# Kernel optimization log

Measured on AMD Instinct MI355X. Metric: run time of the kernel, lower is better.

Reference implementation:

```python
import jax, jax.numpy as jnp
import numpy as np

B, S, H = 1, 2048, 2048
HD, NQ, NKV = 128, 16, 4
FFH = 8192
EPS = 1e-5
ROPE_BASE = 10000.0
SOFTMAX_CAP = 50.0
CLIP_L, CLIP_R = 0.0, 1.0


def setup_inputs() -> dict:
    key = jax.random.key(0)
    ks = jax.random.split(key, 10)
    std = 0.02
    return {
        "x": jax.random.normal(ks[0], (B, S, H), dtype=jnp.float32),
        "attn_norm_w": jax.random.uniform(ks[1], (H,), minval=-1.0, maxval=1.0, dtype=jnp.float32),
        "mlp_norm_w": jax.random.uniform(ks[2], (H,), minval=-1.0, maxval=1.0, dtype=jnp.float32),
        "wq": jax.random.normal(ks[3], (H, NQ * HD), dtype=jnp.float32) * std,
        "wk": jax.random.normal(ks[4], (H, NKV * HD), dtype=jnp.float32) * std,
        "wv": jax.random.normal(ks[5], (H, NKV * HD), dtype=jnp.float32) * std,
        "wo": jax.random.normal(ks[6], (NQ * HD, H), dtype=jnp.float32) * std,
        "w_gate": jax.random.normal(ks[7], (H, FFH), dtype=jnp.float32) * std,
        "w_up": jax.random.normal(ks[8], (H, FFH), dtype=jnp.float32) * std,
        "w_down": jax.random.normal(ks[9], (FFH, H), dtype=jnp.float32) * std,
    }


def _rms_norm(x, w):
    # GroupRMSNorm with group_size=None -> whole hidden dim
    var = jnp.mean(jnp.square(x), axis=-1, keepdims=True)
    return x * jax.lax.rsqrt(var + EPS) * w


def _rope_cos_sin(seq_len, dim):
    inv_freq = 1.0 / (ROPE_BASE ** (jnp.arange(0, dim, 2, dtype=jnp.float32) / dim))
    t = jnp.arange(seq_len, dtype=jnp.float32)
    freqs = jnp.outer(t, inv_freq)                      # [S, dim/2]
    emb = jnp.concatenate([freqs, freqs], axis=-1)      # [S, dim]
    return jnp.cos(emb), jnp.sin(emb)


def _apply_rope(x, cos, sin):
    # x: [B, S, h, d]; rotate-half (LLaMA-style)
    d = x.shape[-1]
    x1, x2 = x[..., : d // 2], x[..., d // 2 :]
    rot = jnp.concatenate([-x2, x1], axis=-1)
    return x * cos[None, :, None, :] + rot * sin[None, :, None, :]


def _qk_norm(x):
    # per-head RMS norm over head_dim (qk_norm_group_size == head_dim), unit weight
    var = jnp.mean(jnp.square(x), axis=-1, keepdims=True)
    return x * jax.lax.rsqrt(var + EPS)


def reference(x, attn_norm_w, mlp_norm_w, wq, wk, wv, wo, w_gate, w_up, w_down):
    # ---- attention sub-layer ----
    h = _rms_norm(x, attn_norm_w)                                     # [B,S,H]
    q = (h @ wq).reshape(B, S, NQ, HD)
    k = (h @ wk).reshape(B, S, NKV, HD)
    v = (h @ wv).reshape(B, S, NKV, HD)

    cos, sin = _rope_cos_sin(S, HD)
    q = _apply_rope(q, cos, sin)
    k = _apply_rope(k, cos, sin)

    q = _qk_norm(q)
    k = _qk_norm(k)

    # GQA: expand kv heads to match q heads
    rep = NQ // NKV
    k = jnp.repeat(k, rep, axis=2)                                    # [B,S,NQ,HD]
    v = jnp.repeat(v, rep, axis=2)

    scale = 1.0 / jnp.sqrt(jnp.float32(HD))
    scores = jnp.einsum("bshd,bthd->bhst", q, k) * scale              # [B,NQ,S,S]
    # softmax cap: cap * tanh(s / cap)
    scores = SOFTMAX_CAP * jnp.tanh(scores / SOFTMAX_CAP)
    causal = jnp.tril(jnp.ones((S, S), dtype=bool))
    scores = jnp.where(causal[None, None], scores, -jnp.inf)
    p = jax.nn.softmax(scores, axis=-1)
    # clip range (l, r): clamp(p * (r - l) + l, 0, 1)
    p = jnp.clip(p * (CLIP_R - CLIP_L) + CLIP_L, 0.0, 1.0)
    o = jnp.einsum("bhst,bthd->bshd", p, v).reshape(B, S, NQ * HD)
    x = x + o @ wo

    # ---- MLP sub-layer (gated SiLU) ----
    h2 = _rms_norm(x, mlp_norm_w)
    mlp_out = (jax.nn.silu(h2 @ w_gate) * (h2 @ w_up)) @ w_down
    return x + mlp_out
```

## Files before the change

kernel.cpp:

```cpp
#include <hip/hip_runtime.h>

typedef __bf16 bf16;
typedef __bf16 bf16x4 __attribute__((ext_vector_type(4)));
typedef __bf16 bf16x8 __attribute__((ext_vector_type(8)));
typedef float f32x4 __attribute__((ext_vector_type(4)));

#define GLP16(gp, lp) __builtin_amdgcn_global_load_lds( \
    (const __attribute__((address_space(1))) void*)(gp), \
    (__attribute__((address_space(3))) void*)(lp), 16, 0, 0)

__device__ __forceinline__ f32x4 mfma16(bf16x8 a, bf16x8 b, f32x4 c) {
    return __builtin_amdgcn_mfma_f32_16x16x32_bf16(a, b, c, 0, 0, 0);
}

__global__ __launch_bounds__(256) void k_rmsnorm(const float* __restrict__ x,
        const float* __restrict__ w, bf16* __restrict__ out) {
    const int H = 2048;
    size_t row = blockIdx.x;
    const float* xr = x + row * H;
    int base = threadIdx.x * 8;
    float4 a = *(const float4*)(xr + base);
    float4 b = *(const float4*)(xr + base + 4);
    float ss = a.x*a.x + a.y*a.y + a.z*a.z + a.w*a.w
             + b.x*b.x + b.y*b.y + b.z*b.z + b.w*b.w;
#pragma unroll
    for (int m = 32; m > 0; m >>= 1) ss += __shfl_xor(ss, m);
    __shared__ float red[4];
    if ((threadIdx.x & 63) == 0) red[threadIdx.x >> 6] = ss;
    __syncthreads();
    float tot = red[0] + red[1] + red[2] + red[3];
    float rs = rsqrtf(tot * (1.0f / H) + 1e-5f);
    float4 wa = *(const float4*)(w + base);
    float4 wb = *(const float4*)(w + base + 4);
    bf16x8 ov;
    ov[0] = (bf16)(a.x * rs * wa.x); ov[1] = (bf16)(a.y * rs * wa.y);
    ov[2] = (bf16)(a.z * rs * wa.z); ov[3] = (bf16)(a.w * rs * wa.w);
    ov[4] = (bf16)(b.x * rs * wb.x); ov[5] = (bf16)(b.y * rs * wb.y);
    ov[6] = (bf16)(b.z * rs * wb.z); ov[7] = (bf16)(b.w * rs * wb.w);
    *(bf16x8*)(out + row * H + base) = ov;
}

__global__ __launch_bounds__(256) void k_convT(const float* __restrict__ W,
        bf16* __restrict__ Wt, int K, int N) {
    __shared__ float t[32][33];
    int k0 = blockIdx.x * 32, n0 = blockIdx.y * 32;
    int tx = threadIdx.x, ty = threadIdx.y;
#pragma unroll
    for (int i = 0; i < 4; i++)
        t[ty + i * 8][tx] = W[(size_t)(k0 + ty + i * 8) * N + n0 + tx];
    __syncthreads();
#pragma unroll
    for (int i = 0; i < 4; i++)
        Wt[(size_t)(n0 + ty + i * 8) * K + k0 + tx] = (bf16)t[tx][ty + i * 8];
}

__global__ __launch_bounds__(256) void k_transpose(const bf16* __restrict__ in,
        bf16* __restrict__ out, int R, int C) {
    __shared__ bf16 t[32][33];
    int r0 = blockIdx.x * 32, c0 = blockIdx.y * 32;
    int tx = threadIdx.x & 31, ty = threadIdx.x >> 5;
#pragma unroll
    for (int i = 0; i < 4; i++)
        t[ty + i * 8][tx] = in[(size_t)(r0 + ty + i * 8) * C + c0 + tx];
    __syncthreads();
#pragma unroll
    for (int i = 0; i < 4; i++)
        out[(size_t)(c0 + ty + i * 8) * R + r0 + tx] = t[tx][ty + i * 8];
}

template<int EPI>
__global__ __launch_bounds__(512, 2) void k_gemm4(const bf16* __restrict__ A,
        const bf16* __restrict__ Bt, void* __restrict__ outp,
        const void* __restrict__ aux, int M, int N, int K, int ksplit) {
    extern __shared__ char lds[];
    const int tid = threadIdx.x, wave = tid >> 6, lane = tid & 63;
    const int lr = lane & 15, kg = lane >> 4;
    const int wm = wave >> 2, wn = wave & 3;
    const int bn = blockIdx.x, bm = blockIdx.y, split = blockIdx.z;
    const int row0 = bm * 256, col0 = bn * 256;
    const int kbeg = split * ksplit;
    const int NT = ksplit >> 6;
    const size_t K2 = (size_t)K * 2;
    const int xorm = (lr & 7) << 4;

    char* const A0 = lds;
    char* const A1 = lds + 32768;
    char* const B0 = lds + 65536;
    char* const B1 = lds + 98304;

    size_t soff[2];
#pragma unroll
    for (int s = 0; s < 2; s++) {
        int d = s * 8192 + tid * 16;
        int rh = d >> 7, c = d & 127;
        soff[s] = (size_t)rh * K2 + (c ^ ((rh & 7) << 4));
    }
    const char* Ab = (const char*)A + ((size_t)row0 * K + kbeg) * 2;
    const char* Bb = (const char*)Bt + ((size_t)col0 * K + kbeg) * 2;

    auto stA = [&](int t, int mh) {
        const char* src = Ab + (size_t)(mh * 128) * K2 + (size_t)t * 128;
        char* dst = lds + (t & 1) * 32768 + mh * 16384 + wave * 1024;
        GLP16(src + soff[0], dst);
        GLP16(src + soff[1], dst + 8192);
    };
    auto stB = [&](int t, int nh) {
        const char* src = Bb + (size_t)(nh * 128) * K2 + (size_t)t * 128;
        char* dst = lds + 65536 + (t & 1) * 32768 + nh * 16384 + wave * 1024;
        GLP16(src + soff[0], dst);
        GLP16(src + soff[1], dst + 8192);
    };

    f32x4 acc[8][4];
#pragma unroll
    for (int m = 0; m < 8; m++)
#pragma unroll
        for (int n = 0; n < 4; n++) acc[m][n] = (f32x4){0, 0, 0, 0};

    bf16x8 a[8], c0[4], c1[4];
    auto rdA = [&](const char* base, int mh) {
#pragma unroll
        for (int mi = 0; mi < 4; mi++)
#pragma unroll
            for (int kk = 0; kk < 2; kk++) {
                int rh = wm * 64 + mi * 16 + lr;
                int c = (kk * 64 + kg * 16) ^ xorm;
                a[mi * 2 + kk] = *(const bf16x8*)(base + mh * 16384 + rh * 128 + c);
            }
    };
    auto rdB = [&](const char* base, int nh, bf16x8 (&b)[4]) {
#pragma unroll
        for (int nj = 0; nj < 2; nj++)
#pragma unroll
            for (int kk = 0; kk < 2; kk++) {
                int rh = wn * 32 + nj * 16 + lr;
                int c = (kk * 64 + kg * 16) ^ xorm;
                b[nj * 2 + kk] = *(const bf16x8*)(base + nh * 16384 + rh * 128 + c);
            }
    };
    auto mm = [&](int mh, int nh, bf16x8 (&b)[4]) {
#pragma unroll
        for (int mi = 0; mi < 4; mi++)
#pragma unroll
            for (int nj = 0; nj < 2; nj++)
#pragma unroll
                for (int kk = 0; kk < 2; kk++)
                    acc[mh * 4 + mi][nh * 2 + nj] =
                        mfma16(a[mi * 2 + kk], b[nj * 2 + kk],
                               acc[mh * 4 + mi][nh * 2 + nj]);
    };

#define SYNCMM \
    __builtin_amdgcn_sched_barrier(0); \
    __builtin_amdgcn_s_barrier(); \
    asm volatile("s_waitcnt lgkmcnt(0)" ::: "memory"); \
    __builtin_amdgcn_sched_barrier(0); \
    __builtin_amdgcn_s_setprio(1);
#define ENDPH \
    __builtin_amdgcn_s_setprio(0); \
    __builtin_amdgcn_sched_barrier(0); \
    __builtin_amdgcn_s_barrier();

    stA(0, 0); stB(0, 0); stB(0, 1); stA(0, 1);
    stA(1, 0); stB(1, 0); stB(1, 1);
    asm volatile("s_waitcnt vmcnt(6)" ::: "memory");
    __builtin_amdgcn_s_barrier();

    const int NIT = NT >> 1;
    for (int it = 0; it < NIT; ++it) {
        const int t = it * 2;
        const bool more = (t + 2 < NT);
        rdA(A0, 0); rdB(B0, 0, c0);
        stA(t + 1, 1);
        SYNCMM; mm(0, 0, c0); ENDPH;
        rdB(B0, 1, c1);
        if (more) stA(t + 2, 0);
        SYNCMM; mm(0, 1, c1); ENDPH;
        rdA(A0, 1);
        if (more) stB(t + 2, 0);
        SYNCMM; mm(1, 1, c1); ENDPH;
        if (more) stB(t + 2, 1);
        __builtin_amdgcn_sched_barrier(0);
        __builtin_amdgcn_s_barrier();
        __builtin_amdgcn_s_setprio(1);
        mm(1, 0, c0);
        __builtin_amdgcn_s_setprio(0);
        if (more) asm volatile("s_waitcnt vmcnt(6)" ::: "memory");
        else      asm volatile("s_waitcnt vmcnt(0)" ::: "memory");
        __builtin_amdgcn_sched_barrier(0);
        __builtin_amdgcn_s_barrier();
        rdA(A1, 0); rdB(B1, 0, c0);
        if (more) stA(t + 2, 1);
        SYNCMM; mm(0, 0, c0); ENDPH;
        rdB(B1, 1, c1);
        if (t + 3 < NT) stA(t + 3, 0);
        SYNCMM; mm(0, 1, c1); ENDPH;
        rdA(A1, 1);
        if (t + 3 < NT) stB(t + 3, 0);
        SYNCMM; mm(1, 1, c1); ENDPH;
        if (t + 3 < NT) stB(t + 3, 1);
        __builtin_amdgcn_sched_barrier(0);
        __builtin_amdgcn_s_barrier();
        __builtin_amdgcn_s_setprio(1);
        mm(1, 0, c0);
        __builtin_amdgcn_s_setprio(0);
        if (more) asm volatile("s_waitcnt vmcnt(6)" ::: "memory");
        __builtin_amdgcn_sched_barrier(0);
        __builtin_amdgcn_s_barrier();
    }
#undef SYNCMM
#undef ENDPH

#pragma unroll
    for (int mi = 0; mi < 8; mi++)
#pragma unroll
        for (int ni = 0; ni < 4; ni++)
#pragma unroll
            for (int r = 0; r < 4; r++) {
                size_t row = row0 + (mi >> 2) * 128 + wm * 64 + (mi & 3) * 16 + kg * 4 + r;
                size_t col = col0 + (ni >> 1) * 128 + wn * 32 + (ni & 1) * 16 + lr;
                size_t idx = row * N + col;
                float vv = acc[mi][ni][r];
                if (EPI == 0) {
                    ((bf16*)outp)[idx] = (bf16)vv;
                } else if (EPI == 2) {
                    float g = (float)((const bf16*)aux)[idx];
                    float sg = g / (1.0f + __expf(-g));
                    ((bf16*)outp)[idx] = (bf16)(sg * vv);
                } else {
                    ((float*)outp)[(size_t)split * M * N + idx] = vv;
                }
            }
}

__global__ __launch_bounds__(256) void k_reduce(const float* __restrict__ parts,
        const float* __restrict__ resid, float* __restrict__ out,
        int ns, size_t n4) {
    size_t i = (size_t)blockIdx.x * 256 + threadIdx.x;
    if (i >= n4) return;
    float4 acc = ((const float4*)resid)[i];
    for (int s = 0; s < ns; s++) {
        float4 p = ((const float4*)(parts + (size_t)s * n4 * 4))[i];
        acc.x += p.x; acc.y += p.y; acc.z += p.z; acc.w += p.w;
    }
    ((float4*)out)[i] = acc;
}

__global__ __launch_bounds__(256) void k_reduce_rms(const float* __restrict__ parts,
        const float* __restrict__ resid, const float* __restrict__ w,
        float* __restrict__ x2, bf16* __restrict__ hb, int ns) {
    const int H = 2048;
    size_t row = blockIdx.x;
    int base = threadIdx.x * 8;
    const float* rr = resid + row * H + base;
    float4 a = *(const float4*)rr;
    float4 b = *(const float4*)(rr + 4);
    for (int s = 0; s < ns; s++) {
        const float* pp = parts + (size_t)s * H * 2048 + row * H + base;
        float4 pa = *(const float4*)pp;
        float4 pb = *(const float4*)(pp + 4);
        a.x += pa.x; a.y += pa.y; a.z += pa.z; a.w += pa.w;
        b.x += pb.x; b.y += pb.y; b.z += pb.z; b.w += pb.w;
    }
    *(float4*)(x2 + row * H + base) = a;
    *(float4*)(x2 + row * H + base + 4) = b;
    float ss = a.x*a.x + a.y*a.y + a.z*a.z + a.w*a.w
             + b.x*b.x + b.y*b.y + b.z*b.z + b.w*b.w;
#pragma unroll
    for (int m = 32; m > 0; m >>= 1) ss += __shfl_xor(ss, m);
    __shared__ float red[4];
    if ((threadIdx.x & 63) == 0) red[threadIdx.x >> 6] = ss;
    __syncthreads();
    float tot = red[0] + red[1] + red[2] + red[3];
    float rs = rsqrtf(tot * (1.0f / H) + 1e-5f);
    float4 wa = *(const float4*)(w + base);
    float4 wb = *(const float4*)(w + base + 4);
    bf16x8 ov;
    ov[0] = (bf16)(a.x * rs * wa.x); ov[1] = (bf16)(a.y * rs * wa.y);
    ov[2] = (bf16)(a.z * rs * wa.z); ov[3] = (bf16)(a.w * rs * wa.w);
    ov[4] = (bf16)(b.x * rs * wb.x); ov[5] = (bf16)(b.y * rs * wb.y);
    ov[6] = (bf16)(b.z * rs * wb.z); ov[7] = (bf16)(b.w * rs * wb.w);
    *(bf16x8*)(hb + row * H + base) = ov;
}

__global__ __launch_bounds__(256) void k_qkvfin(const float* __restrict__ parts,
        bf16* __restrict__ qb, bf16* __restrict__ kb, bf16* __restrict__ vb) {
    int s = blockIdx.x;
    int col = blockIdx.y * 1024 + threadIdx.x * 4;
    const float* p0 = parts + (size_t)s * 3072 + col;
    const float* p1 = p0 + (size_t)2048 * 3072;
    float4 a = *(const float4*)p0;
    float4 b = *(const float4*)p1;
    a.x += b.x; a.y += b.y; a.z += b.z; a.w += b.w;
    bf16x4 o;
    o[0] = (bf16)a.x; o[1] = (bf16)a.y; o[2] = (bf16)a.z; o[3] = (bf16)a.w;
    if (col < 2048)      *(bf16x4*)(qb + (size_t)s * 2048 + col) = o;
    else if (col < 2560) *(bf16x4*)(kb + (size_t)s * 512 + col - 2048) = o;
    else                 *(bf16x4*)(vb + (size_t)s * 512 + col - 2560) = o;
}

__global__ __launch_bounds__(64) void k_rope(bf16* __restrict__ q,
        bf16* __restrict__ k) {
    int s = blockIdx.x, hid = blockIdx.y, lane = threadIdx.x;
    bf16* p;
    if (hid < 16) p = q + (size_t)s * 2048 + hid * 128;
    else          p = k + (size_t)s * 512 + (hid - 16) * 128;
    float x1 = (float)p[lane], x2 = (float)p[lane + 64];
    float f = exp2f((float)lane * -0.2076205059304601f);
    float sn, cs;
    sincosf((float)s * f, &sn, &cs);
    float o1 = x1 * cs - x2 * sn;
    float o2 = x2 * cs + x1 * sn;
    float ss = o1 * o1 + o2 * o2;
#pragma unroll
    for (int m = 32; m > 0; m >>= 1) ss += __shfl_xor(ss, m);
    float rs = rsqrtf(ss * (1.0f / 128.0f) + 1e-5f);
    p[lane] = (bf16)(o1 * rs);
    p[lane + 64] = (bf16)(o2 * rs);
}

__global__ __launch_bounds__(256) void k_attn(const bf16* __restrict__ qg,
        const bf16* __restrict__ kgl, const bf16* __restrict__ vtg,
        bf16* __restrict__ og) {
    extern __shared__ char alds[];
    int pi = blockIdx.x, h = blockIdx.y, kvh = h >> 2;
    int tid = threadIdx.x, wave = tid >> 6, lane = tid & 63;
    int lr = lane & 15, kgrp = lane >> 4;

    int rowQ[4], colQ[4], rowV[4], colV[4];
#pragma unroll
    for (int j = 0; j < 4; j++) {
        int p = j * 4096 + wave * 1024 + lane * 16;
        int ps = p ^ (((p >> 8) & 7) << 4);
        rowQ[j] = ps >> 8; colQ[j] = ps & 255;
        int pv = p ^ (((p >> 7) & 7) << 4);
        rowV[j] = pv >> 7; colV[j] = pv & 127;
    }

    const float C1 = 0.08838834764831845f / 50.0f;
    const float L2E50 = 72.13475204444817f;

#pragma unroll 1
    for (int half = 0; half < 2; ++half) {
        int qt = half ? (31 - pi) : pi;
        int nt = qt + 1;

#pragma unroll
        for (int j = 0; j < 4; j++)
            GLP16((const char*)qg + (size_t)(qt * 64 + rowQ[j]) * 4096 + h * 256 + colQ[j],
                  alds + j * 4096 + wave * 1024);
        for (int t = 0; t < 2 && t < nt; t++) {
#pragma unroll
            for (int j = 0; j < 4; j++)
                GLP16((const char*)kgl + (size_t)(t * 64 + rowQ[j]) * 1024 + kvh * 256 + colQ[j],
                      alds + 16384 + t * 16384 + j * 4096 + wave * 1024);
#pragma unroll
            for (int j = 0; j < 4; j++)
                GLP16((const char*)vtg + (size_t)(kvh * 128 + rowV[j]) * 4096 + t * 128 + colV[j],
                      alds + 49152 + t * 16384 + j * 4096 + wave * 1024);
        }
        if (nt > 1) asm volatile("s_waitcnt vmcnt(8)" ::: "memory");
        else        asm volatile("s_waitcnt vmcnt(0)" ::: "memory");
        __builtin_amdgcn_s_barrier();

        bf16x8 qf[4];
#pragma unroll
        for (int c = 0; c < 4; c++) {
            int b = (wave * 16 + lr) * 256 + c * 64 + kgrp * 16;
            qf[c] = *(const bf16x8*)(alds + (b ^ (((b >> 8) & 7) << 4)));
        }
        f32x4 accO[8];
#pragma unroll
        for (int n = 0; n < 8; n++) accO[n] = (f32x4){0, 0, 0, 0};
        float lsum[4] = {0, 0, 0, 0};
        int qrow = qt * 64 + wave * 16 + kgrp * 4;

        for (int kt = 0; kt < nt; kt++) {
            int buf = kt & 1;
            const char* Kb = alds + 16384 + buf * 16384;
            const char* Vb = alds + 49152 + buf * 16384;
            char* Pb = alds + 81920;
#pragma unroll
            for (int j = 0; j < 4; j++) {
                f32x4 s = {0, 0, 0, 0};
#pragma unroll
                for (int c = 0; c < 4; c++) {
                    int b = (j * 16 + lr) * 256 + c * 64 + kgrp * 16;
                    bf16x8 kf = *(const bf16x8*)(Kb + (b ^ (((b >> 8) & 7) << 4)));
                    s = mfma16(qf[c], kf, s);
                }
                int key = kt * 64 + j * 16 + lr;
#pragma unroll
                for (int r = 0; r < 4; r++) {
                    float y = s[r] * C1;
                    float y2 = y * y;
                    float u = fmaf(y2, 0.13333333f, -0.33333333f);
                    u = fmaf(y2, u, 1.0f);
                    float t5 = y * u;
                    float pe = fmaf(t5, L2E50, -L2E50);
                    float pv = (key <= qrow + r) ? exp2f(pe) : 0.0f;
                    lsum[r] += pv;
                    int wb = (wave * 16 + kgrp * 4 + r) * 128 + (j * 16 + lr) * 2;
                    *(bf16*)(Pb + (wb ^ (((wb >> 7) & 7) << 4))) = (bf16)pv;
                }
            }
            bf16x8 pf[2];
#pragma unroll
            for (int ks2 = 0; ks2 < 2; ks2++) {
                int b = (wave * 16 + lr) * 128 + ks2 * 64 + kgrp * 16;
                pf[ks2] = *(const bf16x8*)(Pb + (b ^ (((b >> 7) & 7) << 4)));
            }
#pragma unroll
            for (int n = 0; n < 8; n++)
#pragma unroll
                for (int ks2 = 0; ks2 < 2; ks2++) {
                    int b = (n * 16 + lr) * 128 + ks2 * 64 + kgrp * 16;
                    bf16x8 vf = *(const bf16x8*)(Vb + (b ^ (((b >> 7) & 7) << 4)));
                    accO[n] = mfma16(pf[ks2], vf, accO[n]);
                }
            __builtin_amdgcn_s_barrier();
            bool more = (kt + 2 < nt);
            if (more) {
                int t = kt + 2;
#pragma unroll
                for (int j = 0; j < 4; j++)
                    GLP16((const char*)kgl + (size_t)(t * 64 + rowQ[j]) * 1024 + kvh * 256 + colQ[j],
                          alds + 16384 + buf * 16384 + j * 4096 + wave * 1024);
#pragma unroll
                for (int j = 0; j < 4; j++)
                    GLP16((const char*)vtg + (size_t)(kvh * 128 + rowV[j]) * 4096 + t * 128 + colV[j],
                          alds + 49152 + buf * 16384 + j * 4096 + wave * 1024);
            }
            if (kt + 1 < nt) {
                if (more) asm volatile("s_waitcnt vmcnt(8)" ::: "memory");
                else      asm volatile("s_waitcnt vmcnt(0)" ::: "memory");
                __builtin_amdgcn_s_barrier();
            }
        }
#pragma unroll
        for (int r = 0; r < 4; r++) {
            float t = lsum[r];
            t += __shfl_xor(t, 1); t += __shfl_xor(t, 2);
            t += __shfl_xor(t, 4); t += __shfl_xor(t, 8);
            lsum[r] = t;
        }
#pragma unroll
        for (int n = 0; n < 8; n++)
#pragma unroll
            for (int r = 0; r < 4; r++) {
                size_t row = qt * 64 + wave * 16 + kgrp * 4 + r;
                og[row * 2048 + h * 128 + n * 16 + lr] = (bf16)(accO[n][r] / lsum[r]);
            }
    }
}

extern "C" void kernel_launch(void* const* d_in, const int* in_sizes, int n_in,
                              void* d_out, int out_size, void* d_ws, size_t ws_size,
                              hipStream_t stream) {
    const float* x      = (const float*)d_in[0];
    const float* attn_w = (const float*)d_in[1];
    const float* mlp_w  = (const float*)d_in[2];
    const float* wq     = (const float*)d_in[3];
    const float* wk     = (const float*)d_in[4];
    const float* wv     = (const float*)d_in[5];
    const float* wo     = (const float*)d_in[6];
    const float* wgate  = (const float*)d_in[7];
    const float* wup    = (const float*)d_in[8];
    const float* wdown  = (const float*)d_in[9];
    float* out = (float*)d_out;
    char* ws = (char*)d_ws;

    const size_t MB = 1024 * 1024;
    bf16* W1  = (bf16*)(ws + 0);
    bf16* W2  = (bf16*)(ws + 32 * MB);
    bf16* W3  = (bf16*)(ws + 64 * MB);
    bf16* hb  = (bf16*)(ws + 96 * MB);
    bf16* qb  = (bf16*)(ws + 104 * MB);
    bf16* kb  = (bf16*)(ws + 112 * MB);
    bf16* vb  = (bf16*)(ws + 114 * MB);
    bf16* ob  = (bf16*)(ws + 116 * MB);
    float* x2 = (float*)(ws + 124 * MB);
    bf16* gb  = (bf16*)(ws + 140 * MB);
    bf16* vt  = (bf16*)(ws + 0);
    float* parts = (float*)(ws + 0);
    float* partsq = (float*)(ws + 116 * MB);

    const int LDS4 = 131072;
    hipFuncSetAttribute((const void*)&k_gemm4<0>,
        hipFuncAttributeMaxDynamicSharedMemorySize, LDS4);
    hipFuncSetAttribute((const void*)&k_gemm4<2>,
        hipFuncAttributeMaxDynamicSharedMemorySize, LDS4);
    hipFuncSetAttribute((const void*)&k_gemm4<3>,
        hipFuncAttributeMaxDynamicSharedMemorySize, LDS4);
    const int LDSA = 90112;
    hipFuncSetAttribute((const void*)&k_attn,
        hipFuncAttributeMaxDynamicSharedMemorySize, LDSA);

    dim3 cb(32, 8);
    const size_t n4 = (size_t)2048 * 2048 / 4;

    k_rmsnorm<<<2048, 256, 0, stream>>>(x, attn_w, hb);
    k_convT<<<dim3(64, 64), cb, 0, stream>>>(wq, W1, 2048, 2048);
    k_convT<<<dim3(64, 16), cb, 0, stream>>>(wk, W1 + 4194304, 2048, 512);
    k_convT<<<dim3(64, 16), cb, 0, stream>>>(wv, W1 + 5242880, 2048, 512);
    k_gemm4<3><<<dim3(12, 8, 2), 512, LDS4, stream>>>(hb, W1, partsq, nullptr,
                                                      2048, 3072, 2048, 1024);
    k_qkvfin<<<dim3(2048, 3), 256, 0, stream>>>(partsq, qb, kb, vb);
    k_transpose<<<dim3(64, 16), 256, 0, stream>>>(vb, vt, 2048, 512);
    k_rope<<<dim3(2048, 20), 64, 0, stream>>>(qb, kb);
    k_attn<<<dim3(16, 16), 256, LDSA, stream>>>(qb, kb, vt, ob);
    k_convT<<<dim3(64, 64), cb, 0, stream>>>(wo, W2, 2048, 2048);
    k_gemm4<3><<<dim3(8, 8, 2), 512, LDS4, stream>>>(ob, W2, parts, nullptr,
                                                     2048, 2048, 2048, 1024);
    k_reduce_rms<<<2048, 256, 0, stream>>>(parts, x, mlp_w, x2, hb, 2);
    k_convT<<<dim3(64, 256), cb, 0, stream>>>(wgate, W1, 2048, 8192);
    k_gemm4<0><<<dim3(32, 8, 1), 512, LDS4, stream>>>(hb, W1, gb, nullptr,
                                                      2048, 8192, 2048, 2048);
    k_convT<<<dim3(64, 256), cb, 0, stream>>>(wup, W2, 2048, 8192);
    k_gemm4<2><<<dim3(32, 8, 1), 512, LDS4, stream>>>(hb, W2, gb, gb,
                                                      2048, 8192, 2048, 2048);
    k_convT<<<dim3(256, 64), cb, 0, stream>>>(wdown, W3, 8192, 2048);
    k_gemm4<3><<<dim3(8, 8, 4), 512, LDS4, stream>>>(gb, W3, parts, nullptr,
                                                     2048, 2048, 8192, 2048);
    k_reduce<<<4096, 256, 0, stream>>>(parts, x2, out, 4, n4);
}
```

Baseline: 473.6 us.

## Fuse gate/up GEMMs via interleaved weights, simplify GEMM barriers, widen rope blocks

Gate and up weights are transposed into one interleaved matrix, so a single GEMM produces both projections and the epilogue pairs adjacent lanes to apply SiLU(gate)*up. This removes the second GEMM's separate A-pass and the bf16 gate round-trip through memory. The GEMM main loop drops the per-phase lgkmcnt waits and sched barriers in favour of plain compiler-fenced barriers, which relies on the compiler inserting the needed LDS waits. The output-projection split-K goes from 2 to 4, and rope runs four heads per 256-thread block instead of one head per 64-thread block.

```diff
diff --git a/kernel.cpp b/kernel.cpp
--- a/kernel.cpp
+++ b/kernel.cpp
@@ -41,7 +41,7 @@
 }
 
 __global__ __launch_bounds__(256) void k_convT(const float* __restrict__ W,
-        bf16* __restrict__ Wt, int K, int N) {
+        bf16* __restrict__ Wt, int K, int N, int rmul, int roff) {
     __shared__ float t[32][33];
     int k0 = blockIdx.x * 32, n0 = blockIdx.y * 32;
     int tx = threadIdx.x, ty = threadIdx.y;
@@ -51,7 +51,8 @@
     __syncthreads();
 #pragma unroll
     for (int i = 0; i < 4; i++)
-        Wt[(size_t)(n0 + ty + i * 8) * K + k0 + tx] = (bf16)t[tx][ty + i * 8];
+        Wt[((size_t)(n0 + ty + i * 8) * rmul + roff) * K + k0 + tx] =
+            (bf16)t[tx][ty + i * 8];
 }
 
 __global__ __launch_bounds__(256) void k_transpose(const bf16* __restrict__ in,
@@ -69,7 +70,7 @@
 }
 
 template<int EPI>
-__global__ __launch_bounds__(512, 2) void k_gemm4(const bf16* __restrict__ A,
+__global__ __launch_bounds__(512, 2) void k_gemm5(const bf16* __restrict__ A,
         const bf16* __restrict__ Bt, void* __restrict__ outp,
         const void* __restrict__ aux, int M, int N, int K, int ksplit) {
     extern __shared__ char lds[];
@@ -83,10 +84,10 @@
     const size_t K2 = (size_t)K * 2;
     const int xorm = (lr & 7) << 4;
 
-    char* const A0 = lds;
-    char* const A1 = lds + 32768;
-    char* const B0 = lds + 65536;
-    char* const B1 = lds + 98304;
+    char* const A0p = lds;
+    char* const A1p = lds + 32768;
+    char* const B0p = lds + 65536;
+    char* const B1p = lds + 98304;
 
     size_t soff[2];
 #pragma unroll
@@ -150,66 +151,54 @@
                                acc[mh * 4 + mi][nh * 2 + nj]);
     };
 
-#define SYNCMM \
-    __builtin_amdgcn_sched_barrier(0); \
-    __builtin_amdgcn_s_barrier(); \
-    asm volatile("s_waitcnt lgkmcnt(0)" ::: "memory"); \
-    __builtin_amdgcn_sched_barrier(0); \
-    __builtin_amdgcn_s_setprio(1);
-#define ENDPH \
-    __builtin_amdgcn_s_setprio(0); \
-    __builtin_amdgcn_sched_barrier(0); \
-    __builtin_amdgcn_s_barrier();
+#define PBAR do { asm volatile("" ::: "memory"); \
+                  __builtin_amdgcn_s_barrier(); \
+                  asm volatile("" ::: "memory"); } while (0)
 
     stA(0, 0); stB(0, 0); stB(0, 1); stA(0, 1);
     stA(1, 0); stB(1, 0); stB(1, 1);
     asm volatile("s_waitcnt vmcnt(6)" ::: "memory");
-    __builtin_amdgcn_s_barrier();
+    PBAR;
 
     const int NIT = NT >> 1;
     for (int it = 0; it < NIT; ++it) {
         const int t = it * 2;
         const bool more = (t + 2 < NT);
-        rdA(A0, 0); rdB(B0, 0, c0);
+        rdA(A0p, 0); rdB(B0p, 0, c0);
         stA(t + 1, 1);
-        SYNCMM; mm(0, 0, c0); ENDPH;
-        rdB(B0, 1, c1);
+        __builtin_amdgcn_s_setprio(1); mm(0, 0, c0); __builtin_amdgcn_s_setprio(0);
+        PBAR;
+        rdB(B0p, 1, c1);
         if (more) stA(t + 2, 0);
-        SYNCMM; mm(0, 1, c1); ENDPH;
-        rdA(A0, 1);
+        __builtin_amdgcn_s_setprio(1); mm(0, 1, c1); __builtin_amdgcn_s_setprio(0);
+        PBAR;
+        rdA(A0p, 1);
         if (more) stB(t + 2, 0);
-        SYNCMM; mm(1, 1, c1); ENDPH;
+        __builtin_amdgcn_s_setprio(1); mm(1, 1, c1); __builtin_amdgcn_s_setprio(0);
+        PBAR;
         if (more) stB(t + 2, 1);
-        __builtin_amdgcn_sched_barrier(0);
-        __builtin_amdgcn_s_barrier();
-        __builtin_amdgcn_s_setprio(1);
-        mm(1, 0, c0);
-        __builtin_amdgcn_s_setprio(0);
+        __builtin_amdgcn_s_setprio(1); mm(1, 0, c0); __builtin_amdgcn_s_setprio(0);
         if (more) asm volatile("s_waitcnt vmcnt(6)" ::: "memory");
         else      asm volatile("s_waitcnt vmcnt(0)" ::: "memory");
-        __builtin_amdgcn_sched_barrier(0);
-        __builtin_amdgcn_s_barrier();
-        rdA(A1, 0); rdB(B1, 0, c0);
+        PBAR;
+        rdA(A1p, 0); rdB(B1p, 0, c0);
         if (more) stA(t + 2, 1);
-        SYNCMM; mm(0, 0, c0); ENDPH;
-        rdB(B1, 1, c1);
+        __builtin_amdgcn_s_setprio(1); mm(0, 0, c0); __builtin_amdgcn_s_setprio(0);
+        PBAR;
+        rdB(B1p, 1, c1);
         if (t + 3 < NT) stA(t + 3, 0);
-        SYNCMM; mm(0, 1, c1); ENDPH;
-        rdA(A1, 1);
+        __builtin_amdgcn_s_setprio(1); mm(0, 1, c1); __builtin_amdgcn_s_setprio(0);
+        PBAR;
+        rdA(A1p, 1);
         if (t + 3 < NT) stB(t + 3, 0);
-        SYNCMM; mm(1, 1, c1); ENDPH;
+        __builtin_amdgcn_s_setprio(1); mm(1, 1, c1); __builtin_amdgcn_s_setprio(0);
+        PBAR;
         if (t + 3 < NT) stB(t + 3, 1);
-        __builtin_amdgcn_sched_barrier(0);
-        __builtin_amdgcn_s_barrier();
-        __builtin_amdgcn_s_setprio(1);
-        mm(1, 0, c0);
-        __builtin_amdgcn_s_setprio(0);
+        __builtin_amdgcn_s_setprio(1); mm(1, 0, c0); __builtin_amdgcn_s_setprio(0);
         if (more) asm volatile("s_waitcnt vmcnt(6)" ::: "memory");
-        __builtin_amdgcn_sched_barrier(0);
-        __builtin_amdgcn_s_barrier();
+        PBAR;
     }
-#undef SYNCMM
-#undef ENDPH
+#undef PBAR
 
 #pragma unroll
     for (int mi = 0; mi < 8; mi++)
@@ -219,16 +208,17 @@
             for (int r = 0; r < 4; r++) {
                 size_t row = row0 + (mi >> 2) * 128 + wm * 64 + (mi & 3) * 16 + kg * 4 + r;
                 size_t col = col0 + (ni >> 1) * 128 + wn * 32 + (ni & 1) * 16 + lr;
-                size_t idx = row * N + col;
                 float vv = acc[mi][ni][r];
-                if (EPI == 0) {
-                    ((bf16*)outp)[idx] = (bf16)vv;
-                } else if (EPI == 2) {
-                    float g = (float)((const bf16*)aux)[idx];
+                if (EPI == 3) {
+                    ((float*)outp)[(size_t)split * M * N + row * N + col] = vv;
+                } else {
+                    float pv = __shfl_xor(vv, 1);
+                    float g = (lane & 1) ? pv : vv;
+                    float u = (lane & 1) ? vv : pv;
                     float sg = g / (1.0f + __expf(-g));
-                    ((bf16*)outp)[idx] = (bf16)(sg * vv);
-                } else {
-                    ((float*)outp)[(size_t)split * M * N + idx] = vv;
+                    if (!(lane & 1))
+                        ((bf16*)outp)[row * (size_t)(N >> 1) + (col >> 1)] =
+                            (bf16)(sg * u);
                 }
             }
 }
@@ -299,9 +289,10 @@
     else                 *(bf16x4*)(vb + (size_t)s * 512 + col - 2560) = o;
 }
 
-__global__ __launch_bounds__(64) void k_rope(bf16* __restrict__ q,
+__global__ __launch_bounds__(256) void k_rope(bf16* __restrict__ q,
         bf16* __restrict__ k) {
-    int s = blockIdx.x, hid = blockIdx.y, lane = threadIdx.x;
+    int s = blockIdx.x, lane = threadIdx.x & 63;
+    int hid = blockIdx.y * 4 + (threadIdx.x >> 6);
     bf16* p;
     if (hid < 16) p = q + (size_t)s * 2048 + hid * 128;
     else          p = k + (size_t)s * 512 + (hid - 16) * 128;
@@ -471,27 +462,27 @@
     char* ws = (char*)d_ws;
 
     const size_t MB = 1024 * 1024;
-    bf16* W1  = (bf16*)(ws + 0);
-    bf16* W2  = (bf16*)(ws + 32 * MB);
-    bf16* W3  = (bf16*)(ws + 64 * MB);
-    bf16* hb  = (bf16*)(ws + 96 * MB);
-    bf16* qb  = (bf16*)(ws + 104 * MB);
-    bf16* kb  = (bf16*)(ws + 112 * MB);
-    bf16* vb  = (bf16*)(ws + 114 * MB);
-    bf16* ob  = (bf16*)(ws + 116 * MB);
-    float* x2 = (float*)(ws + 124 * MB);
-    bf16* gb  = (bf16*)(ws + 140 * MB);
-    bf16* vt  = (bf16*)(ws + 0);
-    float* parts = (float*)(ws + 0);
-    float* partsq = (float*)(ws + 116 * MB);
-
-    const int LDS4 = 131072;
-    hipFuncSetAttribute((const void*)&k_gemm4<0>,
-        hipFuncAttributeMaxDynamicSharedMemorySize, LDS4);
-    hipFuncSetAttribute((const void*)&k_gemm4<2>,
-        hipFuncAttributeMaxDynamicSharedMemorySize, LDS4);
-    hipFuncSetAttribute((const void*)&k_gemm4<3>,
-        hipFuncAttributeMaxDynamicSharedMemorySize, LDS4);
+    bf16* Wqkv = (bf16*)(ws + 0);
+    bf16* vt   = (bf16*)(ws + 0);
+    float* pO  = (float*)(ws + 0);
+    bf16* Wgu  = (bf16*)(ws + 0);
+    float* pD  = (float*)(ws + 0);
+    bf16* WoT  = (bf16*)(ws + 64 * MB);
+    bf16* WdT  = (bf16*)(ws + 64 * MB);
+    bf16* hb   = (bf16*)(ws + 96 * MB);
+    bf16* qb   = (bf16*)(ws + 104 * MB);
+    bf16* kb   = (bf16*)(ws + 112 * MB);
+    bf16* vb   = (bf16*)(ws + 114 * MB);
+    bf16* ob   = (bf16*)(ws + 116 * MB);
+    float* x2  = (float*)(ws + 124 * MB);
+    bf16* gb   = (bf16*)(ws + 140 * MB);
+    float* pQ  = (float*)(ws + 116 * MB);
+
+    const int LDS5 = 131072;
+    hipFuncSetAttribute((const void*)&k_gemm5<3>,
+        hipFuncAttributeMaxDynamicSharedMemorySize, LDS5);
+    hipFuncSetAttribute((const void*)&k_gemm5<4>,
+        hipFuncAttributeMaxDynamicSharedMemorySize, LDS5);
     const int LDSA = 90112;
     hipFuncSetAttribute((const void*)&k_attn,
         hipFuncAttributeMaxDynamicSharedMemorySize, LDSA);
@@ -500,27 +491,25 @@
     const size_t n4 = (size_t)2048 * 2048 / 4;
 
     k_rmsnorm<<<2048, 256, 0, stream>>>(x, attn_w, hb);
-    k_convT<<<dim3(64, 64), cb, 0, stream>>>(wq, W1, 2048, 2048);
-    k_convT<<<dim3(64, 16), cb, 0, stream>>>(wk, W1 + 4194304, 2048, 512);
-    k_convT<<<dim3(64, 16), cb, 0, stream>>>(wv, W1 + 5242880, 2048, 512);
-    k_gemm4<3><<<dim3(12, 8, 2), 512, LDS4, stream>>>(hb, W1, partsq, nullptr,
+    k_convT<<<dim3(64, 64), cb, 0, stream>>>(wq, Wqkv, 2048, 2048, 1, 0);
+    k_convT<<<dim3(64, 16), cb, 0, stream>>>(wk, Wqkv + 4194304, 2048, 512, 1, 0);
+    k_convT<<<dim3(64, 16), cb, 0, stream>>>(wv, Wqkv + 5242880, 2048, 512, 1, 0);
+    k_gemm5<3><<<dim3(12, 8, 2), 512, LDS5, stream>>>(hb, Wqkv, pQ, nullptr,
                                                       2048, 3072, 2048, 1024);
-    k_qkvfin<<<dim3(2048, 3), 256, 0, stream>>>(partsq, qb, kb, vb);
+    k_qkvfin<<<dim3(2048, 3), 256, 0, stream>>>(pQ, qb, kb, vb);
     k_transpose<<<dim3(64, 16), 256, 0, stream>>>(vb, vt, 2048, 512);
-    k_rope<<<dim3(2048, 20), 64, 0, stream>>>(qb, kb);
+    k_rope<<<dim3(2048, 5), 256, 0, stream>>>(qb, kb);
     k_attn<<<dim3(16, 16), 256, LDSA, stream>>>(qb, kb, vt, ob);
-    k_convT<<<dim3(64, 64), cb, 0, stream>>>(wo, W2, 2048, 2048);
-    k_gemm4<3><<<dim3(8, 8, 2), 512, LDS4, stream>>>(ob, W2, parts, nullptr,
-                                                     2048, 2048, 2048, 1024);
-    k_reduce_rms<<<2048, 256, 0, stream>>>(parts, x, mlp_w, x2, hb, 2);
-    k_convT<<<dim3(64, 256), cb, 0, stream>>>(wgate, W1, 2048, 8192);
-    k_gemm4<0><<<dim3(32, 8, 1), 512, LDS4, stream>>>(hb, W1, gb, nullptr,
-                                                      2048, 8192, 2048, 2048);
-    k_convT<<<dim3(64, 256), cb, 0, stream>>>(wup, W2, 2048, 8192);
-    k_gemm4<2><<<dim3(32, 8, 1), 512, LDS4, stream>>>(hb, W2, gb, gb,
-                                                      2048, 8192, 2048, 2048);
-    k_convT<<<dim3(256, 64), cb, 0, stream>>>(wdown, W3, 8192, 2048);
-    k_gemm4<3><<<dim3(8, 8, 4), 512, LDS4, stream>>>(gb, W3, parts, nullptr,
+    k_convT<<<dim3(64, 64), cb, 0, stream>>>(wo, WoT, 2048, 2048, 1, 0);
+    k_gemm5<3><<<dim3(8, 8, 4), 512, LDS5, stream>>>(ob, WoT, pO, nullptr,
+                                                     2048, 2048, 2048, 512);
+    k_reduce_rms<<<2048, 256, 0, stream>>>(pO, x, mlp_w, x2, hb, 4);
+    k_convT<<<dim3(64, 256), cb, 0, stream>>>(wgate, Wgu, 2048, 8192, 2, 0);
+    k_convT<<<dim3(64, 256), cb, 0, stream>>>(wup, Wgu, 2048, 8192, 2, 1);
+    k_gemm5<4><<<dim3(64, 8, 1), 512, LDS5, stream>>>(hb, Wgu, gb, nullptr,
+                                                      2048, 16384, 2048, 2048);
+    k_convT<<<dim3(256, 64), cb, 0, stream>>>(wdown, WdT, 8192, 2048, 1, 0);
+    k_gemm5<3><<<dim3(8, 8, 4), 512, LDS5, stream>>>(gb, WdT, pD, nullptr,
                                                      2048, 2048, 8192, 2048);
-    k_reduce<<<4096, 256, 0, stream>>>(parts, x2, out, 4, n4);
-}
+    k_reduce<<<4096, 256, 0, stream>>>(pD, x2, out, 4, n4);
+}
```

Measured after the change: 467.0 us. Within noise of the previous version (-1.4%).
